# Optimization experiments

Measured on AMD Instinct MI355X. Metric: run time of the kernel, lower is better.

The kernel has to match this reference:

```python
import jax, jax.numpy as jnp
import numpy as np

# Capsule layer dims (from original CapsNet paper, per module docstring)
O = 10      # n_out_capsules
U = 36      # n_in_capsules_unique (6*6)
S = 32      # n_in_capsules_sharing_per_unique
E = 16      # n_out_features
F = 8       # n_in_features
N = U * S   # n_in_capsules = 1152
ITERS = 3   # n_iterations
B = 256     # batch size


def squash(v, axis):
    norm = jnp.linalg.norm(v, axis=axis, keepdims=True)
    return v * norm / (1.0 + norm ** 2)


def setup_inputs() -> dict:
    key = jax.random.key(0)
    k1, k2 = jax.random.split(key)
    x = jax.random.normal(k1, (B, N, F), dtype=jnp.float32)
    scale = np.float32(np.sqrt(2.0 / (N * F + O * E)))
    # weights: (n_out_capsules, n_in_capsules_unique, n_out_features, n_in_features)
    W = jax.random.normal(k2, (O, U, E, F), dtype=jnp.float32) * scale
    return {"x": x, "W": W}


def reference(x, W):
    b_sz = x.shape[0]
    xs = x.reshape(b_sz, U, S, F)
    # transform: shared weight over the S sharing dim -> (B, O, U, S, E)
    u = jnp.einsum('ouef,busf->bouse', W, xs).reshape(b_sz, O, N, E)
    u_hat = jax.lax.stop_gradient(u)

    b = jnp.zeros((b_sz, O, N), dtype=x.dtype)
    c = jax.nn.softmax(b, axis=1)  # uniform over output capsules
    for _ in range(ITERS):
        # v: (B, O, 1, E)
        v = squash(jnp.sum(c[..., None] * u_hat, axis=2, keepdims=True), axis=3)
        # agreement: (B, O, N)
        b = b + jnp.sum(u_hat * v, axis=3)
        c = jax.nn.softmax(b, axis=1)

    # final pass uses non-detached u so gradients flow through transform
    out = squash(jnp.sum(c[..., None] * u, axis=2, keepdims=True), axis=3)
    return out.reshape(b_sz, O, E)
```

## Files before the change

### kernel.cpp

```cpp
#include <hip/hip_runtime.h>
#include <math.h>


namespace {

constexpr int kO = 10;
constexpr int kU = 36;
constexpr int kS = 32;
constexpr int kE = 16;
constexpr int kF = 8;
constexpr int kN = kU * kS;
constexpr int kIters = 3;
constexpr int kThreads = 512;
constexpr int kPitch = 12;

__launch_bounds__(kThreads, 2)
__global__ void caps_routing_kernel(const float* __restrict__ xg,
                                    const float* __restrict__ Wg,
                                    float* __restrict__ outg) {
  __shared__ float s_x[kN * kF];
  __shared__ float s_c[kO * kN];
  __shared__ float s_cx[kO * kU * kPitch];
  __shared__ float s_wv[kO * kU * kPitch];
  __shared__ float s_vp[kO * kE * 3];
  __shared__ float s_sx[kU * kF];

  const int t = threadIdx.x;
  const int w = t >> 6;
  const int l = t & 63;
  const int b = blockIdx.x;

  float xr0[kF], xr1[kF], xr2[kF];
  float br0[kO], br1[kO], br2[kO];
  const bool has3 = (w < 4) && (l < 32);

  const int u0r = t >> 5;
  const int s0r = t & 31;
  const int rot0 = (s0r + u0r) & 31;
  const int u1r = 16 + (t >> 5);
  const int rot1 = (s0r + u1r) & 31;
  const int u2r = 32 + w;
  const int rot2 = (l + u2r) & 31;

#define STAGEROW(XR, N, U, S)                                                 \
  {                                                                           \
    const float4* src_ =                                                      \
        reinterpret_cast<const float4*>(xg + ((size_t)b * kN + (N)) * kF);    \
    const float4 a0_ = src_[0];                                               \
    const float4 a1_ = src_[1];                                               \
    XR[0] = a0_.x; XR[1] = a0_.y; XR[2] = a0_.z; XR[3] = a0_.w;               \
    XR[4] = a1_.x; XR[5] = a1_.y; XR[6] = a1_.z; XR[7] = a1_.w;               \
    const int sl0_ = (((S) << 1) + (U)) & 63;                                 \
    const int sl1_ = (((S) << 1) + 1 + (U)) & 63;                             \
    *reinterpret_cast<float4*>(&s_x[(U) * 256 + sl0_ * 4]) = a0_;             \
    *reinterpret_cast<float4*>(&s_x[(U) * 256 + sl1_ * 4]) = a1_;             \
    float4 r0_ = a0_, r1_ = a1_;                                              \
    _Pragma("unroll")                                                         \
    for (int m_ = 1; m_ <= 16; m_ <<= 1) {                                    \
      r0_.x += __shfl_xor(r0_.x, m_); r0_.y += __shfl_xor(r0_.y, m_);         \
      r0_.z += __shfl_xor(r0_.z, m_); r0_.w += __shfl_xor(r0_.w, m_);         \
      r1_.x += __shfl_xor(r1_.x, m_); r1_.y += __shfl_xor(r1_.y, m_);         \
      r1_.z += __shfl_xor(r1_.z, m_); r1_.w += __shfl_xor(r1_.w, m_);         \
    }                                                                         \
    if ((S) == 0) {                                                           \
      *reinterpret_cast<float4*>(&s_sx[(U) * kF + 0]) = r0_;                  \
      *reinterpret_cast<float4*>(&s_sx[(U) * kF + 4]) = r1_;                  \
    }                                                                         \
  }

  STAGEROW(xr0, t, u0r, s0r)
  STAGEROW(xr1, t + 512, u1r, s0r)
  if (has3) STAGEROW(xr2, 1024 + w * 32 + l, u2r, l)
#undef STAGEROW
#pragma unroll
  for (int o = 0; o < kO; ++o) { br0[o] = 0.f; br1[o] = 0.f; br2[o] = 0.f; }
  __syncthreads();

  for (int it = 0; it <= kIters; ++it) {
    if (it > 0) {
      if (l < 46) {
        const int i = w * 46 + l;
        if (i < 360) {
          const int op  = i / 72;
          const int rem = i - op * 72;
          const int u   = rem >> 1;
          const int h   = rem & 1;
          const int o0  = op * 2, o1 = o0 + 1;
          float4 p00 = make_float4(0.f, 0.f, 0.f, 0.f);
          float4 p01 = make_float4(0.f, 0.f, 0.f, 0.f);
          float4 p10 = make_float4(0.f, 0.f, 0.f, 0.f);
          float4 p11 = make_float4(0.f, 0.f, 0.f, 0.f);
#pragma unroll 4
          for (int j = 0; j < 16; ++j) {
            const int s   = h * 16 + j;
            const int rot = (s + u) & 31;
            const int sl0 = ((s << 1) + u) & 63;
            const int sl1 = ((s << 1) + 1 + u) & 63;
            const float4 xa =
                *reinterpret_cast<const float4*>(&s_x[u * 256 + sl0 * 4]);
            const float4 xb =
                *reinterpret_cast<const float4*>(&s_x[u * 256 + sl1 * 4]);
            const float c0 = s_c[o0 * kN + u * 32 + rot];
            const float c1 = s_c[o1 * kN + u * 32 + rot];
            p00.x += c0 * xa.x; p00.y += c0 * xa.y; p00.z += c0 * xa.z; p00.w += c0 * xa.w;
            p01.x += c0 * xb.x; p01.y += c0 * xb.y; p01.z += c0 * xb.z; p01.w += c0 * xb.w;
            p10.x += c1 * xa.x; p10.y += c1 * xa.y; p10.z += c1 * xa.z; p10.w += c1 * xa.w;
            p11.x += c1 * xb.x; p11.y += c1 * xb.y; p11.z += c1 * xb.z; p11.w += c1 * xb.w;
          }
          p00.x += __shfl_xor(p00.x, 1); p00.y += __shfl_xor(p00.y, 1);
          p00.z += __shfl_xor(p00.z, 1); p00.w += __shfl_xor(p00.w, 1);
          p01.x += __shfl_xor(p01.x, 1); p01.y += __shfl_xor(p01.y, 1);
          p01.z += __shfl_xor(p01.z, 1); p01.w += __shfl_xor(p01.w, 1);
          p10.x += __shfl_xor(p10.x, 1); p10.y += __shfl_xor(p10.y, 1);
          p10.z += __shfl_xor(p10.z, 1); p10.w += __shfl_xor(p10.w, 1);
          p11.x += __shfl_xor(p11.x, 1); p11.y += __shfl_xor(p11.y, 1);
          p11.z += __shfl_xor(p11.z, 1); p11.w += __shfl_xor(p11.w, 1);
          if (h == 0) {
            float4* d = reinterpret_cast<float4*>(&s_cx[(o0 * kU + u) * kPitch]);
            d[0] = p00; d[1] = p01;
          } else {
            float4* d = reinterpret_cast<float4*>(&s_cx[(o1 * kU + u) * kPitch]);
            d[0] = p10; d[1] = p11;
          }
        }
      }
      __syncthreads();
    }

    if (l < 60) {
      const int i  = w * 60 + l;
      const int o  = i / 48;
      const int r  = i - o * 48;
      const int e  = r / 3;
      const int uc = r - e * 3;
      const int u0 = uc * 12;
      float accA = 0.f, accB = 0.f;
      const float* wrow = Wg + ((size_t)(o * kU + u0) * kE + e) * kF;
      if (it == 0) {
#pragma unroll 4
        for (int ui = 0; ui < 12; ++ui) {
          const float4* wp = reinterpret_cast<const float4*>(wrow);
          const float4 w0 = wp[0];
          const float4 w1 = wp[1];
          const float4* cp =
              reinterpret_cast<const float4*>(&s_sx[(u0 + ui) * kF]);
          const float4 c0 = cp[0];
          const float4 c1 = cp[1];
          accA += w0.x * c0.x + w0.y * c0.y + w0.z * c0.z + w0.w * c0.w;
          accB += w1.x * c1.x + w1.y * c1.y + w1.z * c1.z + w1.w * c1.w;
          wrow += kE * kF;
        }
        accA = (accA + accB) * 0.1f;
      } else {
#pragma unroll 4
        for (int ui = 0; ui < 12; ++ui) {
          const float4* wp = reinterpret_cast<const float4*>(wrow);
          const float4 w0 = wp[0];
          const float4 w1 = wp[1];
          const float4* cp = reinterpret_cast<const float4*>(
              &s_cx[(o * kU + u0 + ui) * kPitch]);
          const float4 c0 = cp[0];
          const float4 c1 = cp[1];
          accA += w0.x * c0.x + w0.y * c0.y + w0.z * c0.z + w0.w * c0.w;
          accB += w1.x * c1.x + w1.y * c1.y + w1.z * c1.z + w1.w * c1.w;
          wrow += kE * kF;
        }
        accA += accB;
      }
      s_vp[(o * kE + e) * 3 + uc] = accA;
    }
    __syncthreads();

    if (it == kIters) {
      if (t < kO * kE) {
        const float vsum = s_vp[t * 3 + 0] + s_vp[t * 3 + 1] + s_vp[t * 3 + 2];
        float n2 = vsum * vsum;
#pragma unroll
        for (int m = 1; m <= 8; m <<= 1) n2 += __shfl_xor(n2, m);
        const float scale = sqrtf(n2) / (1.f + n2);
        outg[(size_t)b * kO * kE + t] = vsum * scale;
      }
      break;
    }

    if (l < 45) {
      const int i = w * 45 + l;
      const int o = i / 36;
      const int u = i - o * 36;
#define SUMVP(E_) (s_vp[(o * kE + (E_)) * 3 + 0] + \
                   s_vp[(o * kE + (E_)) * 3 + 1] + \
                   s_vp[(o * kE + (E_)) * 3 + 2])
      float4 va, vb, vc, vd;
      va.x = SUMVP(0);  va.y = SUMVP(1);  va.z = SUMVP(2);  va.w = SUMVP(3);
      vb.x = SUMVP(4);  vb.y = SUMVP(5);  vb.z = SUMVP(6);  vb.w = SUMVP(7);
      vc.x = SUMVP(8);  vc.y = SUMVP(9);  vc.z = SUMVP(10); vc.w = SUMVP(11);
      vd.x = SUMVP(12); vd.y = SUMVP(13); vd.z = SUMVP(14); vd.w = SUMVP(15);
#undef SUMVP
      const float n2 =
          va.x * va.x + va.y * va.y + va.z * va.z + va.w * va.w +
          vb.x * vb.x + vb.y * vb.y + vb.z * vb.z + vb.w * vb.w +
          vc.x * vc.x + vc.y * vc.y + vc.z * vc.z + vc.w * vc.w +
          vd.x * vd.x + vd.y * vd.y + vd.z * vd.z + vd.w * vd.w;
      const float scale = sqrtf(n2) / (1.f + n2);
      const float* wbase = Wg + (size_t)(o * kU + u) * kE * kF;
      float4 acc0 = make_float4(0.f, 0.f, 0.f, 0.f);
      float4 acc1 = make_float4(0.f, 0.f, 0.f, 0.f);
#define WSTEP(VE_, E_)                                                        \
  {                                                                           \
    const float4* wp = reinterpret_cast<const float4*>(wbase + (E_) * kF);    \
    const float4 w0 = wp[0];                                                  \
    const float4 w1 = wp[1];                                                  \
    const float ve = (VE_) * scale;                                           \
    acc0.x += ve * w0.x; acc0.y += ve * w0.y;                                 \
    acc0.z += ve * w0.z; acc0.w += ve * w0.w;                                 \
    acc1.x += ve * w1.x; acc1.y += ve * w1.y;                                 \
    acc1.z += ve * w1.z; acc1.w += ve * w1.w;                                 \
  }
      WSTEP(va.x, 0)  WSTEP(va.y, 1)  WSTEP(va.z, 2)  WSTEP(va.w, 3)
      WSTEP(vb.x, 4)  WSTEP(vb.y, 5)  WSTEP(vb.z, 6)  WSTEP(vb.w, 7)
      WSTEP(vc.x, 8)  WSTEP(vc.y, 9)  WSTEP(vc.z, 10) WSTEP(vc.w, 11)
      WSTEP(vd.x, 12) WSTEP(vd.y, 13) WSTEP(vd.z, 14) WSTEP(vd.w, 15)
#undef WSTEP
      float4* d = reinterpret_cast<float4*>(&s_wv[(o * kU + u) * kPitch]);
      d[0] = acc0;
      d[1] = acc1;
    }
    __syncthreads();

#define BSMROW(XR, BR, U, ROT)                                                \
  {                                                                           \
    float mx_ = -3.4e38f;                                                     \
    _Pragma("unroll")                                                         \
    for (int o_ = 0; o_ < kO; ++o_) {                                         \
      const float4* wp_ =                                                     \
          reinterpret_cast<const float4*>(&s_wv[(o_ * kU + (U)) * kPitch]);   \
      const float4 w0_ = wp_[0];                                              \
      const float4 w1_ = wp_[1];                                              \
      BR[o_] += w0_.x * XR[0] + w0_.y * XR[1] + w0_.z * XR[2] + w0_.w * XR[3] \
              + w1_.x * XR[4] + w1_.y * XR[5] + w1_.z * XR[6] + w1_.w * XR[7];\
      mx_ = fmaxf(mx_, BR[o_]);                                               \
    }                                                                         \
    float ex_[kO];                                                            \
    float sum_ = 0.f;                                                         \
    _Pragma("unroll")                                                         \
    for (int o_ = 0; o_ < kO; ++o_) {                                         \
      ex_[o_] = __expf(BR[o_] - mx_);                                         \
      sum_ += ex_[o_];                                                        \
    }                                                                         \
    const float inv_ = 1.f / sum_;                                            \
    _Pragma("unroll")                                                         \
    for (int o_ = 0; o_ < kO; ++o_)                                           \
      s_c[o_ * kN + (U) * 32 + (ROT)] = ex_[o_] * inv_;                       \
  }
    BSMROW(xr0, br0, u0r, rot0)
    BSMROW(xr1, br1, u1r, rot1)
    if (has3) BSMROW(xr2, br2, u2r, rot2)
#undef BSMROW
    __syncthreads();
  }
}

}

extern "C" void kernel_launch(void* const* d_in, const int* in_sizes, int n_in,
                              void* d_out, int out_size, void* d_ws, size_t ws_size,
                              hipStream_t stream) {
  const float* x = (const float*)d_in[0];
  const float* W = (const float*)d_in[1];
  float* out = (float*)d_out;

  const int batch = in_sizes[0] / (kN * kF);
  caps_routing_kernel<<<dim3(batch), dim3(kThreads), 0, stream>>>(x, W, out);
}
```

Before: 105.4 us.

## Double block to 1024 threads and redistribute routing work across more wavefronts

Raises the block size from 512 to 1024 threads so each thread holds fewer input capsule rows (two instead of three) and the per-phase work (c·x reduction, W·v projection, W·wv transform) is split finer across 16 wavefronts. The v computation now splits u into four chunks reduced with shuffles instead of three partials in shared memory, and the wv step splits the E dimension across lane pairs. This shortens the per-thread serial work per phase but adds shuffle reductions and doubles the threads synchronising at each barrier. With 256 blocks, the larger block size may also limit how many blocks fit per CU.

Result: slower. 121.8 us (+15.6%).

```diff
diff --git a/kernel.cpp b/kernel.cpp
--- a/kernel.cpp
+++ b/kernel.cpp
@@ -11,10 +11,10 @@
 constexpr int kF = 8;
 constexpr int kN = kU * kS;
 constexpr int kIters = 3;
-constexpr int kThreads = 512;
+constexpr int kThreads = 1024;
 constexpr int kPitch = 12;
 
-__launch_bounds__(kThreads, 2)
+__launch_bounds__(kThreads, 4)
 __global__ void caps_routing_kernel(const float* __restrict__ xg,
                                     const float* __restrict__ Wg,
                                     float* __restrict__ outg) {
@@ -22,7 +22,7 @@
   __shared__ float s_c[kO * kN];
   __shared__ float s_cx[kO * kU * kPitch];
   __shared__ float s_wv[kO * kU * kPitch];
-  __shared__ float s_vp[kO * kE * 3];
+  __shared__ float s_v[kO * kE];
   __shared__ float s_sx[kU * kF];
 
   const int t = threadIdx.x;
@@ -30,17 +30,15 @@
   const int l = t & 63;
   const int b = blockIdx.x;
 
-  float xr0[kF], xr1[kF], xr2[kF];
-  float br0[kO], br1[kO], br2[kO];
-  const bool has3 = (w < 4) && (l < 32);
+  float xr0[kF], xr1[kF];
+  float br0[kO], br1[kO];
+  const bool has2 = (t < 128);
 
   const int u0r = t >> 5;
   const int s0r = t & 31;
   const int rot0 = (s0r + u0r) & 31;
-  const int u1r = 16 + (t >> 5);
+  const int u1r = 32 + (t >> 5);
   const int rot1 = (s0r + u1r) & 31;
-  const int u2r = 32 + w;
-  const int rot2 = (l + u2r) & 31;
 
 #define STAGEROW(XR, N, U, S)                                                 \
   {                                                                           \
@@ -69,81 +67,68 @@
   }
 
   STAGEROW(xr0, t, u0r, s0r)
-  STAGEROW(xr1, t + 512, u1r, s0r)
-  if (has3) STAGEROW(xr2, 1024 + w * 32 + l, u2r, l)
+  if (has2) STAGEROW(xr1, 1024 + t, u1r, s0r)
 #undef STAGEROW
 #pragma unroll
-  for (int o = 0; o < kO; ++o) { br0[o] = 0.f; br1[o] = 0.f; br2[o] = 0.f; }
+  for (int o = 0; o < kO; ++o) { br0[o] = 0.f; br1[o] = 0.f; }
   __syncthreads();
 
   for (int it = 0; it <= kIters; ++it) {
     if (it > 0) {
-      if (l < 46) {
-        const int i = w * 46 + l;
-        if (i < 360) {
-          const int op  = i / 72;
-          const int rem = i - op * 72;
-          const int u   = rem >> 1;
-          const int h   = rem & 1;
-          const int o0  = op * 2, o1 = o0 + 1;
-          float4 p00 = make_float4(0.f, 0.f, 0.f, 0.f);
-          float4 p01 = make_float4(0.f, 0.f, 0.f, 0.f);
-          float4 p10 = make_float4(0.f, 0.f, 0.f, 0.f);
-          float4 p11 = make_float4(0.f, 0.f, 0.f, 0.f);
+      const int base = w * 45 + (w & 1);
+      const int cnt = 46 - ((w & 1) << 1);
+      if (l < cnt) {
+        const int i = base + l;
+        const int o = i / 72;
+        const int rem = i - o * 72;
+        const int u = rem >> 1;
+        const int h = rem & 1;
+        float4 p0 = make_float4(0.f, 0.f, 0.f, 0.f);
+        float4 p1 = make_float4(0.f, 0.f, 0.f, 0.f);
 #pragma unroll 4
-          for (int j = 0; j < 16; ++j) {
-            const int s   = h * 16 + j;
-            const int rot = (s + u) & 31;
-            const int sl0 = ((s << 1) + u) & 63;
-            const int sl1 = ((s << 1) + 1 + u) & 63;
-            const float4 xa =
-                *reinterpret_cast<const float4*>(&s_x[u * 256 + sl0 * 4]);
-            const float4 xb =
-                *reinterpret_cast<const float4*>(&s_x[u * 256 + sl1 * 4]);
-            const float c0 = s_c[o0 * kN + u * 32 + rot];
-            const float c1 = s_c[o1 * kN + u * 32 + rot];
-            p00.x += c0 * xa.x; p00.y += c0 * xa.y; p00.z += c0 * xa.z; p00.w += c0 * xa.w;
-            p01.x += c0 * xb.x; p01.y += c0 * xb.y; p01.z += c0 * xb.z; p01.w += c0 * xb.w;
-            p10.x += c1 * xa.x; p10.y += c1 * xa.y; p10.z += c1 * xa.z; p10.w += c1 * xa.w;
-            p11.x += c1 * xb.x; p11.y += c1 * xb.y; p11.z += c1 * xb.z; p11.w += c1 * xb.w;
-          }
-          p00.x += __shfl_xor(p00.x, 1); p00.y += __shfl_xor(p00.y, 1);
-          p00.z += __shfl_xor(p00.z, 1); p00.w += __shfl_xor(p00.w, 1);
-          p01.x += __shfl_xor(p01.x, 1); p01.y += __shfl_xor(p01.y, 1);
-          p01.z += __shfl_xor(p01.z, 1); p01.w += __shfl_xor(p01.w, 1);
-          p10.x += __shfl_xor(p10.x, 1); p10.y += __shfl_xor(p10.y, 1);
-          p10.z += __shfl_xor(p10.z, 1); p10.w += __shfl_xor(p10.w, 1);
-          p11.x += __shfl_xor(p11.x, 1); p11.y += __shfl_xor(p11.y, 1);
-          p11.z += __shfl_xor(p11.z, 1); p11.w += __shfl_xor(p11.w, 1);
-          if (h == 0) {
-            float4* d = reinterpret_cast<float4*>(&s_cx[(o0 * kU + u) * kPitch]);
-            d[0] = p00; d[1] = p01;
-          } else {
-            float4* d = reinterpret_cast<float4*>(&s_cx[(o1 * kU + u) * kPitch]);
-            d[0] = p10; d[1] = p11;
-          }
+        for (int j = 0; j < 16; ++j) {
+          const int s = h * 16 + j;
+          const int rot = (s + u) & 31;
+          const int sl0 = ((s << 1) + u) & 63;
+          const int sl1 = ((s << 1) + 1 + u) & 63;
+          const float4 xa =
+              *reinterpret_cast<const float4*>(&s_x[u * 256 + sl0 * 4]);
+          const float4 xb =
+              *reinterpret_cast<const float4*>(&s_x[u * 256 + sl1 * 4]);
+          const float c0 = s_c[o * kN + u * 32 + rot];
+          p0.x += c0 * xa.x; p0.y += c0 * xa.y; p0.z += c0 * xa.z; p0.w += c0 * xa.w;
+          p1.x += c0 * xb.x; p1.y += c0 * xb.y; p1.z += c0 * xb.z; p1.w += c0 * xb.w;
+        }
+        p0.x += __shfl_xor(p0.x, 1); p0.y += __shfl_xor(p0.y, 1);
+        p0.z += __shfl_xor(p0.z, 1); p0.w += __shfl_xor(p0.w, 1);
+        p1.x += __shfl_xor(p1.x, 1); p1.y += __shfl_xor(p1.y, 1);
+        p1.z += __shfl_xor(p1.z, 1); p1.w += __shfl_xor(p1.w, 1);
+        if (h == 0) {
+          float4* d = reinterpret_cast<float4*>(&s_cx[(o * kU + u) * kPitch]);
+          d[0] = p0;
+          d[1] = p1;
         }
       }
       __syncthreads();
     }
 
-    if (l < 60) {
-      const int i  = w * 60 + l;
-      const int o  = i / 48;
-      const int r  = i - o * 48;
-      const int e  = r / 3;
-      const int uc = r - e * 3;
-      const int u0 = uc * 12;
+    if (l < 40) {
+      const int i = w * 40 + l;
+      const int g = i >> 2;
+      const int uc = i & 3;
+      const int o = g >> 4;
+      const int e = g & 15;
+      const int u0 = uc * 9;
       float accA = 0.f, accB = 0.f;
       const float* wrow = Wg + ((size_t)(o * kU + u0) * kE + e) * kF;
       if (it == 0) {
-#pragma unroll 4
-        for (int ui = 0; ui < 12; ++ui) {
+#pragma unroll
+        for (int j = 0; j < 9; ++j) {
           const float4* wp = reinterpret_cast<const float4*>(wrow);
           const float4 w0 = wp[0];
           const float4 w1 = wp[1];
           const float4* cp =
-              reinterpret_cast<const float4*>(&s_sx[(u0 + ui) * kF]);
+              reinterpret_cast<const float4*>(&s_sx[(u0 + j) * kF]);
           const float4 c0 = cp[0];
           const float4 c1 = cp[1];
           accA += w0.x * c0.x + w0.y * c0.y + w0.z * c0.z + w0.w * c0.w;
@@ -152,13 +137,13 @@
         }
         accA = (accA + accB) * 0.1f;
       } else {
-#pragma unroll 4
-        for (int ui = 0; ui < 12; ++ui) {
+#pragma unroll
+        for (int j = 0; j < 9; ++j) {
           const float4* wp = reinterpret_cast<const float4*>(wrow);
           const float4 w0 = wp[0];
           const float4 w1 = wp[1];
           const float4* cp = reinterpret_cast<const float4*>(
-              &s_cx[(o * kU + u0 + ui) * kPitch]);
+              &s_cx[(o * kU + u0 + j) * kPitch]);
           const float4 c0 = cp[0];
           const float4 c1 = cp[1];
           accA += w0.x * c0.x + w0.y * c0.y + w0.z * c0.z + w0.w * c0.w;
@@ -167,13 +152,15 @@
         }
         accA += accB;
       }
-      s_vp[(o * kE + e) * 3 + uc] = accA;
+      accA += __shfl_xor(accA, 1);
+      accA += __shfl_xor(accA, 2);
+      if ((l & 3) == 0) s_v[g] = accA;
     }
     __syncthreads();
 
     if (it == kIters) {
       if (t < kO * kE) {
-        const float vsum = s_vp[t * 3 + 0] + s_vp[t * 3 + 1] + s_vp[t * 3 + 2];
+        const float vsum = s_v[t];
         float n2 = vsum * vsum;
 #pragma unroll
         for (int m = 1; m <= 8; m <<= 1) n2 += __shfl_xor(n2, m);
@@ -183,31 +170,39 @@
       break;
     }
 
-    if (l < 45) {
-      const int i = w * 45 + l;
-      const int o = i / 36;
-      const int u = i - o * 36;
-#define SUMVP(E_) (s_vp[(o * kE + (E_)) * 3 + 0] + \
-                   s_vp[(o * kE + (E_)) * 3 + 1] + \
-                   s_vp[(o * kE + (E_)) * 3 + 2])
-      float4 va, vb, vc, vd;
-      va.x = SUMVP(0);  va.y = SUMVP(1);  va.z = SUMVP(2);  va.w = SUMVP(3);
-      vb.x = SUMVP(4);  vb.y = SUMVP(5);  vb.z = SUMVP(6);  vb.w = SUMVP(7);
-      vc.x = SUMVP(8);  vc.y = SUMVP(9);  vc.z = SUMVP(10); vc.w = SUMVP(11);
-      vd.x = SUMVP(12); vd.y = SUMVP(13); vd.z = SUMVP(14); vd.w = SUMVP(15);
-#undef SUMVP
-      const float n2 =
-          va.x * va.x + va.y * va.y + va.z * va.z + va.w * va.w +
-          vb.x * vb.x + vb.y * vb.y + vb.z * vb.z + vb.w * vb.w +
-          vc.x * vc.x + vc.y * vc.y + vc.z * vc.z + vc.w * vc.w +
-          vd.x * vd.x + vd.y * vd.y + vd.z * vd.z + vd.w * vd.w;
-      const float scale = sqrtf(n2) / (1.f + n2);
-      const float* wbase = Wg + (size_t)(o * kU + u) * kE * kF;
-      float4 acc0 = make_float4(0.f, 0.f, 0.f, 0.f);
-      float4 acc1 = make_float4(0.f, 0.f, 0.f, 0.f);
-#define WSTEP(VE_, E_)                                                        \
+    {
+      const int base = w * 45 + (w & 1);
+      const int cnt = 46 - ((w & 1) << 1);
+      if (l < cnt) {
+        const int i = base + l;
+        const int g = i >> 1;
+        const int eh = i & 1;
+        const int o = g / 36;
+        const int u = g - o * 36;
+        float4 va, vb, vc, vd;
+        va.x = s_v[o * kE + 0];  va.y = s_v[o * kE + 1];
+        va.z = s_v[o * kE + 2];  va.w = s_v[o * kE + 3];
+        vb.x = s_v[o * kE + 4];  vb.y = s_v[o * kE + 5];
+        vb.z = s_v[o * kE + 6];  vb.w = s_v[o * kE + 7];
+        vc.x = s_v[o * kE + 8];  vc.y = s_v[o * kE + 9];
+        vc.z = s_v[o * kE + 10]; vc.w = s_v[o * kE + 11];
+        vd.x = s_v[o * kE + 12]; vd.y = s_v[o * kE + 13];
+        vd.z = s_v[o * kE + 14]; vd.w = s_v[o * kE + 15];
+        const float n2 =
+            va.x * va.x + va.y * va.y + va.z * va.z + va.w * va.w +
+            vb.x * vb.x + vb.y * vb.y + vb.z * vb.z + vb.w * vb.w +
+            vc.x * vc.x + vc.y * vc.y + vc.z * vc.z + vc.w * vc.w +
+            vd.x * vd.x + vd.y * vd.y + vd.z * vd.z + vd.w * vd.w;
+        const float scale = sqrtf(n2) / (1.f + n2);
+        const float4 h0 = eh ? vc : va;
+        const float4 h1 = eh ? vd : vb;
+        const float* wbase =
+            Wg + ((size_t)(o * kU + u) * kE + eh * 8) * kF;
+        float4 acc0 = make_float4(0.f, 0.f, 0.f, 0.f);
+        float4 acc1 = make_float4(0.f, 0.f, 0.f, 0.f);
+#define WSTEP(VE_, K_)                                                        \
   {                                                                           \
-    const float4* wp = reinterpret_cast<const float4*>(wbase + (E_) * kF);    \
+    const float4* wp = reinterpret_cast<const float4*>(wbase + (K_) * kF);    \
     const float4 w0 = wp[0];                                                  \
     const float4 w1 = wp[1];                                                  \
     const float ve = (VE_) * scale;                                           \
@@ -216,16 +211,21 @@
     acc1.x += ve * w1.x; acc1.y += ve * w1.y;                                 \
     acc1.z += ve * w1.z; acc1.w += ve * w1.w;                                 \
   }
-      WSTEP(va.x, 0)  WSTEP(va.y, 1)  WSTEP(va.z, 2)  WSTEP(va.w, 3)
-      WSTEP(vb.x, 4)  WSTEP(vb.y, 5)  WSTEP(vb.z, 6)  WSTEP(vb.w, 7)
-      WSTEP(vc.x, 8)  WSTEP(vc.y, 9)  WSTEP(vc.z, 10) WSTEP(vc.w, 11)
-      WSTEP(vd.x, 12) WSTEP(vd.y, 13) WSTEP(vd.z, 14) WSTEP(vd.w, 15)
+        WSTEP(h0.x, 0) WSTEP(h0.y, 1) WSTEP(h0.z, 2) WSTEP(h0.w, 3)
+        WSTEP(h1.x, 4) WSTEP(h1.y, 5) WSTEP(h1.z, 6) WSTEP(h1.w, 7)
 #undef WSTEP
-      float4* d = reinterpret_cast<float4*>(&s_wv[(o * kU + u) * kPitch]);
-      d[0] = acc0;
-      d[1] = acc1;
-    }
-    __syncthreads();
+        acc0.x += __shfl_xor(acc0.x, 1); acc0.y += __shfl_xor(acc0.y, 1);
+        acc0.z += __shfl_xor(acc0.z, 1); acc0.w += __shfl_xor(acc0.w, 1);
+        acc1.x += __shfl_xor(acc1.x, 1); acc1.y += __shfl_xor(acc1.y, 1);
+        acc1.z += __shfl_xor(acc1.z, 1); acc1.w += __shfl_xor(acc1.w, 1);
+        if (eh == 0) {
+          float4* d = reinterpret_cast<float4*>(&s_wv[(o * kU + u) * kPitch]);
+          d[0] = acc0;
+          d[1] = acc1;
+        }
+      }
+      __syncthreads();
+    }
 
 #define BSMROW(XR, BR, U, ROT)                                                \
   {                                                                           \
@@ -253,8 +253,7 @@
       s_c[o_ * kN + (U) * 32 + (ROT)] = ex_[o_] * inv_;                       \
   }
     BSMROW(xr0, br0, u0r, rot0)
-    BSMROW(xr1, br1, u1r, rot1)
-    if (has3) BSMROW(xr2, br2, u2r, rot2)
+    if (has2) BSMROW(xr1, br1, u1r, rot1)
 #undef BSMROW
     __syncthreads();
   }
```

## Partition capsules per wave so routing phases sync within waves instead of blocks

Applied to the files above, without the earlier changes.

Reassigns input-capsule ownership so each wave owns a fixed set of unique capsules (4 or 5). The W·v projection, the softmax update and the c·x reduction for those capsules run inside the same wave, so two block-wide barriers per iteration become wave-local LDS waits. The c·x accumulation moves to the end of each iteration and runs per owned capsule. This cuts block synchronization but leaves the work unevenly spread across waves, and each lane now does longer serial loops.

Measured after the change: 105.6 us. About the same (+0.2%).

```diff
diff --git a/kernel.cpp b/kernel.cpp
--- a/kernel.cpp
+++ b/kernel.cpp
@@ -13,6 +13,13 @@
 constexpr int kIters = 3;
 constexpr int kThreads = 512;
 constexpr int kPitch = 12;
+
+#define WAVESYNC()                                              \
+  do {                                                          \
+    __builtin_amdgcn_wave_barrier();                            \
+    asm volatile("s_waitcnt lgkmcnt(0)" ::: "memory");          \
+    __builtin_amdgcn_wave_barrier();                            \
+  } while (0)
 
 __launch_bounds__(kThreads, 2)
 __global__ void caps_routing_kernel(const float* __restrict__ xg,
@@ -30,17 +37,20 @@
   const int l = t & 63;
   const int b = blockIdx.x;
 
-  float xr0[kF], xr1[kF], xr2[kF];
-  float br0[kO], br1[kO], br2[kO];
-  const bool has3 = (w < 4) && (l < 32);
+  const bool five = (w >= 2 && w < 6);
+  const int nu = five ? 5 : 4;
+  const bool has3 = five && (l < 32);
 
   const int u0r = t >> 5;
   const int s0r = t & 31;
   const int rot0 = (s0r + u0r) & 31;
   const int u1r = 16 + (t >> 5);
   const int rot1 = (s0r + u1r) & 31;
-  const int u2r = 32 + w;
+  const int u2r = 30 + w;
   const int rot2 = (l + u2r) & 31;
+
+  float xr0[kF], xr1[kF], xr2[kF];
+  float br0[kO], br1[kO], br2[kO];
 
 #define STAGEROW(XR, N, U, S)                                                 \
   {                                                                           \
@@ -70,68 +80,20 @@
 
   STAGEROW(xr0, t, u0r, s0r)
   STAGEROW(xr1, t + 512, u1r, s0r)
-  if (has3) STAGEROW(xr2, 1024 + w * 32 + l, u2r, l)
+  if (has3) STAGEROW(xr2, 1024 + (w - 2) * 32 + l, u2r, l)
 #undef STAGEROW
 #pragma unroll
   for (int o = 0; o < kO; ++o) { br0[o] = 0.f; br1[o] = 0.f; br2[o] = 0.f; }
   __syncthreads();
 
+#define UOFJ(J) ((J) < 2 ? 2 * w + (J) : ((J) < 4 ? 14 + 2 * w + (J) : 30 + w))
+
   for (int it = 0; it <= kIters; ++it) {
-    if (it > 0) {
-      if (l < 46) {
-        const int i = w * 46 + l;
-        if (i < 360) {
-          const int op  = i / 72;
-          const int rem = i - op * 72;
-          const int u   = rem >> 1;
-          const int h   = rem & 1;
-          const int o0  = op * 2, o1 = o0 + 1;
-          float4 p00 = make_float4(0.f, 0.f, 0.f, 0.f);
-          float4 p01 = make_float4(0.f, 0.f, 0.f, 0.f);
-          float4 p10 = make_float4(0.f, 0.f, 0.f, 0.f);
-          float4 p11 = make_float4(0.f, 0.f, 0.f, 0.f);
-#pragma unroll 4
-          for (int j = 0; j < 16; ++j) {
-            const int s   = h * 16 + j;
-            const int rot = (s + u) & 31;
-            const int sl0 = ((s << 1) + u) & 63;
-            const int sl1 = ((s << 1) + 1 + u) & 63;
-            const float4 xa =
-                *reinterpret_cast<const float4*>(&s_x[u * 256 + sl0 * 4]);
-            const float4 xb =
-                *reinterpret_cast<const float4*>(&s_x[u * 256 + sl1 * 4]);
-            const float c0 = s_c[o0 * kN + u * 32 + rot];
-            const float c1 = s_c[o1 * kN + u * 32 + rot];
-            p00.x += c0 * xa.x; p00.y += c0 * xa.y; p00.z += c0 * xa.z; p00.w += c0 * xa.w;
-            p01.x += c0 * xb.x; p01.y += c0 * xb.y; p01.z += c0 * xb.z; p01.w += c0 * xb.w;
-            p10.x += c1 * xa.x; p10.y += c1 * xa.y; p10.z += c1 * xa.z; p10.w += c1 * xa.w;
-            p11.x += c1 * xb.x; p11.y += c1 * xb.y; p11.z += c1 * xb.z; p11.w += c1 * xb.w;
-          }
-          p00.x += __shfl_xor(p00.x, 1); p00.y += __shfl_xor(p00.y, 1);
-          p00.z += __shfl_xor(p00.z, 1); p00.w += __shfl_xor(p00.w, 1);
-          p01.x += __shfl_xor(p01.x, 1); p01.y += __shfl_xor(p01.y, 1);
-          p01.z += __shfl_xor(p01.z, 1); p01.w += __shfl_xor(p01.w, 1);
-          p10.x += __shfl_xor(p10.x, 1); p10.y += __shfl_xor(p10.y, 1);
-          p10.z += __shfl_xor(p10.z, 1); p10.w += __shfl_xor(p10.w, 1);
-          p11.x += __shfl_xor(p11.x, 1); p11.y += __shfl_xor(p11.y, 1);
-          p11.z += __shfl_xor(p11.z, 1); p11.w += __shfl_xor(p11.w, 1);
-          if (h == 0) {
-            float4* d = reinterpret_cast<float4*>(&s_cx[(o0 * kU + u) * kPitch]);
-            d[0] = p00; d[1] = p01;
-          } else {
-            float4* d = reinterpret_cast<float4*>(&s_cx[(o1 * kU + u) * kPitch]);
-            d[0] = p10; d[1] = p11;
-          }
-        }
-      }
-      __syncthreads();
-    }
-
     if (l < 60) {
-      const int i  = w * 60 + l;
-      const int o  = i / 48;
-      const int r  = i - o * 48;
-      const int e  = r / 3;
+      const int i = w * 60 + l;
+      const int o = i / 48;
+      const int r = i - o * 48;
+      const int e = r / 3;
       const int uc = r - e * 3;
       const int u0 = uc * 12;
       float accA = 0.f, accB = 0.f;
@@ -183,10 +145,12 @@
       break;
     }
 
-    if (l < 45) {
-      const int i = w * 45 + l;
-      const int o = i / 36;
-      const int u = i - o * 36;
+
+    if (l < 40) {
+      const int o = l % 10;
+      const int q = l / 10;
+      const int fh = q & 1;
+      const int jp = q >> 1;
 #define SUMVP(E_) (s_vp[(o * kE + (E_)) * 3 + 0] + \
                    s_vp[(o * kE + (E_)) * 3 + 1] + \
                    s_vp[(o * kE + (E_)) * 3 + 2])
@@ -202,30 +166,32 @@
           vc.x * vc.x + vc.y * vc.y + vc.z * vc.z + vc.w * vc.w +
           vd.x * vd.x + vd.y * vd.y + vd.z * vd.z + vd.w * vd.w;
       const float scale = sqrtf(n2) / (1.f + n2);
-      const float* wbase = Wg + (size_t)(o * kU + u) * kE * kF;
-      float4 acc0 = make_float4(0.f, 0.f, 0.f, 0.f);
-      float4 acc1 = make_float4(0.f, 0.f, 0.f, 0.f);
+      va.x *= scale; va.y *= scale; va.z *= scale; va.w *= scale;
+      vb.x *= scale; vb.y *= scale; vb.z *= scale; vb.w *= scale;
+      vc.x *= scale; vc.y *= scale; vc.z *= scale; vc.w *= scale;
+      vd.x *= scale; vd.y *= scale; vd.z *= scale; vd.w *= scale;
+      for (int j = jp; j < nu; j += 2) {
+        const int u = UOFJ(j);
+        const float* wbase =
+            Wg + (size_t)((o * kU + u) * kE) * kF + fh * 4;
+        float4 acc = make_float4(0.f, 0.f, 0.f, 0.f);
 #define WSTEP(VE_, E_)                                                        \
   {                                                                           \
-    const float4* wp = reinterpret_cast<const float4*>(wbase + (E_) * kF);    \
-    const float4 w0 = wp[0];                                                  \
-    const float4 w1 = wp[1];                                                  \
-    const float ve = (VE_) * scale;                                           \
-    acc0.x += ve * w0.x; acc0.y += ve * w0.y;                                 \
-    acc0.z += ve * w0.z; acc0.w += ve * w0.w;                                 \
-    acc1.x += ve * w1.x; acc1.y += ve * w1.y;                                 \
-    acc1.z += ve * w1.z; acc1.w += ve * w1.w;                                 \
-  }
-      WSTEP(va.x, 0)  WSTEP(va.y, 1)  WSTEP(va.z, 2)  WSTEP(va.w, 3)
-      WSTEP(vb.x, 4)  WSTEP(vb.y, 5)  WSTEP(vb.z, 6)  WSTEP(vb.w, 7)
-      WSTEP(vc.x, 8)  WSTEP(vc.y, 9)  WSTEP(vc.z, 10) WSTEP(vc.w, 11)
-      WSTEP(vd.x, 12) WSTEP(vd.y, 13) WSTEP(vd.z, 14) WSTEP(vd.w, 15)
+    const float4* wp =                                                        \
+        reinterpret_cast<const float4*>(wbase + (E_) * kF);                   \
+    const float4 w4 = wp[0];                                                  \
+    acc.x += (VE_) * w4.x; acc.y += (VE_) * w4.y;                             \
+    acc.z += (VE_) * w4.z; acc.w += (VE_) * w4.w;                             \
+  }
+        WSTEP(va.x, 0)  WSTEP(va.y, 1)  WSTEP(va.z, 2)  WSTEP(va.w, 3)
+        WSTEP(vb.x, 4)  WSTEP(vb.y, 5)  WSTEP(vb.z, 6)  WSTEP(vb.w, 7)
+        WSTEP(vc.x, 8)  WSTEP(vc.y, 9)  WSTEP(vc.z, 10) WSTEP(vc.w, 11)
+        WSTEP(vd.x, 12) WSTEP(vd.y, 13) WSTEP(vd.z, 14) WSTEP(vd.w, 15)
 #undef WSTEP
-      float4* d = reinterpret_cast<float4*>(&s_wv[(o * kU + u) * kPitch]);
-      d[0] = acc0;
-      d[1] = acc1;
-    }
-    __syncthreads();
+        *reinterpret_cast<float4*>(&s_wv[(o * kU + u) * kPitch + fh * 4]) = acc;
+      }
+    }
+    WAVESYNC();
 
 #define BSMROW(XR, BR, U, ROT)                                                \
   {                                                                           \
@@ -256,8 +222,34 @@
     BSMROW(xr1, br1, u1r, rot1)
     if (has3) BSMROW(xr2, br2, u2r, rot2)
 #undef BSMROW
+    WAVESYNC();
+
+    if (l < nu * 10) {
+      const int o = l % 10;
+      const int j = l / 10;
+      const int u = UOFJ(j);
+      float4 p0 = make_float4(0.f, 0.f, 0.f, 0.f);
+      float4 p1 = make_float4(0.f, 0.f, 0.f, 0.f);
+      const float* cbase = &s_c[o * kN + u * 32];
+      const float* xbase = &s_x[u * 256];
+#pragma unroll 4
+      for (int s = 0; s < kS; ++s) {
+        const int rot = (s + u) & 31;
+        const int sl0 = ((s << 1) + u) & 63;
+        const int sl1 = ((s << 1) + 1 + u) & 63;
+        const float4 xa = *reinterpret_cast<const float4*>(&xbase[sl0 * 4]);
+        const float4 xb = *reinterpret_cast<const float4*>(&xbase[sl1 * 4]);
+        const float c0 = cbase[rot];
+        p0.x += c0 * xa.x; p0.y += c0 * xa.y; p0.z += c0 * xa.z; p0.w += c0 * xa.w;
+        p1.x += c0 * xb.x; p1.y += c0 * xb.y; p1.z += c0 * xb.z; p1.w += c0 * xb.w;
+      }
+      float4* d = reinterpret_cast<float4*>(&s_cx[(o * kU + u) * kPitch]);
+      d[0] = p0;
+      d[1] = p1;
+    }
     __syncthreads();
   }
+#undef UOFJ
 }
 
 }
```
